# Kernel optimization log

Measured on AMD Instinct MI355X. Metric: run time of the kernel, lower is better.

The kernel has to match this reference:

```python
import jax, jax.numpy as jnp
import numpy as np
from jax import lax

B, CIN, COUT, H, W = 4, 32, 64, 192, 192
K = 3  # kernel size
RED = 16  # SE reduction
EPS = 1e-5


def _conv2d_same(x, w, b):
    y = lax.conv_general_dilated(x, w, (1, 1), 'SAME',
                                 dimension_numbers=('NCHW', 'OIHW', 'NCHW'))
    return y + b[None, :, None, None]


def _bilinear_gather(x, py, px):
    # x: [B,C,H,W]; py/px: [B,KK,H,W] absolute sample coords -> [B,C,KK,H,W]
    Bb, C, Hh, Ww = x.shape
    KK = py.shape[1]
    y0 = jnp.floor(py); x0 = jnp.floor(px)
    wy = py - y0; wx = px - x0
    x_flat = x.reshape(Bb, C, Hh * Ww)

    def corner(yi, xi, wgt):
        valid = (yi >= 0) & (yi < Hh) & (xi >= 0) & (xi < Ww)
        yc = jnp.clip(yi, 0, Hh - 1).astype(jnp.int32)
        xc = jnp.clip(xi, 0, Ww - 1).astype(jnp.int32)
        idx = (yc * Ww + xc).reshape(Bb, 1, KK * Hh * Ww)
        g = jnp.take_along_axis(x_flat, idx, axis=2).reshape(Bb, C, KK, Hh, Ww)
        w_eff = (wgt * valid.astype(x.dtype))[:, None]  # [B,1,KK,H,W]
        return g * w_eff

    out = (corner(y0, x0, (1 - wy) * (1 - wx))
           + corner(y0, x0 + 1, (1 - wy) * wx)
           + corner(y0 + 1, x0, wy * (1 - wx))
           + corner(y0 + 1, x0 + 1, wy * wx))
    return out  # [B,C,KK,H,W]


def _deform_conv(x, offsets, w, b):
    # torchvision DeformConv2d, stride 1, pad 1, dilation 1, 1 offset group.
    Bb, C, Hh, Ww = x.shape
    off = offsets.reshape(Bb, K * K, 2, Hh, Ww)
    dy, dx = off[:, :, 0], off[:, :, 1]  # [B,KK,H,W]
    ky, kx = jnp.meshgrid(jnp.arange(K) - 1, jnp.arange(K) - 1, indexing='ij')
    hg, wg = jnp.meshgrid(jnp.arange(Hh), jnp.arange(Ww), indexing='ij')
    py = hg[None, None] + ky.reshape(-1)[None, :, None, None] + dy
    px = wg[None, None] + kx.reshape(-1)[None, :, None, None] + dx
    sampled = _bilinear_gather(x, py, px)  # [B,CIN,KK,H,W]
    y = jnp.einsum('bckhw,ock->bohw', sampled, w.reshape(w.shape[0], C, K * K))
    return y + b[None, :, None, None]


def _forward(x, w_off, b_off, w_def, b_def, bn_gamma, bn_beta,
             fc1_w, fc1_b, fc2_w, fc2_b):
    offsets = _conv2d_same(x, w_off, b_off)
    y = _deform_conv(x, offsets, w_def, b_def)
    # BatchNorm2d (training-mode batch statistics)
    mean = jnp.mean(y, axis=(0, 2, 3), keepdims=True)
    var = jnp.var(y, axis=(0, 2, 3), keepdims=True)
    y = (y - mean) * lax.rsqrt(var + EPS)
    y = y * bn_gamma[None, :, None, None] + bn_beta[None, :, None, None]
    # SE layer
    s = jnp.mean(y, axis=(2, 3))  # [B,C]
    s = jax.nn.relu(s @ fc1_w.T + fc1_b)
    s = jax.nn.sigmoid(s @ fc2_w.T + fc2_b)
    y = y * s[:, :, None, None]
    y = jax.nn.relu(y)
    # MaxPool 2x2 stride 2
    y = lax.reduce_window(y, -jnp.inf, lax.max, (1, 1, 2, 2), (1, 1, 2, 2), 'VALID')
    return y


def setup_inputs() -> dict:
    key = jax.random.key(0)
    ks = jax.random.split(key, 12)
    rn = lambda k, s, sc=1.0: (jax.random.normal(k, s, dtype=jnp.float32) * sc)
    return {
        'x': rn(ks[0], (B, CIN, H, W)),
        'w_off': rn(ks[1], (2 * K * K, CIN, K, K), 0.02),
        'b_off': jnp.zeros((2 * K * K,), jnp.float32),
        'w_def': rn(ks[2], (COUT, CIN, K, K), 0.05),
        'b_def': rn(ks[3], (COUT,), 0.05),
        'bn_gamma': jnp.ones((COUT,), jnp.float32),
        'bn_beta': jnp.zeros((COUT,), jnp.float32),
        'fc1_w': rn(ks[4], (COUT // RED, COUT), 0.1),
        'fc1_b': jnp.zeros((COUT // RED,), jnp.float32),
        'fc2_w': rn(ks[5], (COUT, COUT // RED), 0.1),
        'fc2_b': jnp.zeros((COUT,), jnp.float32),
    }


def reference(x, w_off, b_off, w_def, b_def, bn_gamma, bn_beta,
              fc1_w, fc1_b, fc2_w, fc2_b):
    return _forward(x, w_off, b_off, w_def, b_def, bn_gamma, bn_beta,
                    fc1_w, fc1_b, fc2_w, fc2_b)
```

## Files before the change

kernel.cpp:

```cpp
#include <hip/hip_runtime.h>
#include <math.h>

#define B_    4
#define CIN_  32
#define COUT_ 64
#define H_    192
#define W_    192
#define HW_   (H_ * W_)
#define NPIX_ (B_ * HW_)
#define EPS_  1e-5f

static __device__ __forceinline__ int swz1152(int blk) {
    return ((blk & 7) * 144) + (blk >> 3);
}

__global__ __launch_bounds__(256) void k_pre(
    const float* __restrict__ x, const float* __restrict__ w_def,
    const float* __restrict__ w_off, float* __restrict__ xt,
    float* __restrict__ wt_def, float* __restrict__ wt_off,
    float* __restrict__ stats)
{
    if (blockIdx.x < NPIX_ / 256) {
        const int pid = blockIdx.x * 256 + threadIdx.x;
        const int b   = pid / HW_;
        const int rem = pid - b * HW_;
        const float* xb = x + (size_t)b * CIN_ * HW_ + rem;
        float4 v[8];
#pragma unroll
        for (int j = 0; j < 8; ++j) {
            v[j].x = xb[(j * 4 + 0) * HW_];
            v[j].y = xb[(j * 4 + 1) * HW_];
            v[j].z = xb[(j * 4 + 2) * HW_];
            v[j].w = xb[(j * 4 + 3) * HW_];
        }
        float4* dst = (float4*)(xt + (size_t)pid * 32);
#pragma unroll
        for (int j = 0; j < 8; ++j) dst[j] = v[j];
    } else {
        const int i = (blockIdx.x - NPIX_ / 256) * 256 + threadIdx.x;
        if (i < 18432) {
            const int o  = i & 63;
            const int c  = (i >> 6) & 31;
            const int kk = i >> 11;
            wt_def[i] = w_def[(o * 32 + c) * 9 + kk];
        } else if (i < 18432 + 5760) {
            const int e  = i - 18432;
            const int o  = e % 20;
            const int t  = e / 20;
            const int c  = t & 31;
            const int kk = t >> 5;
            wt_off[e] = (o < 18) ? w_off[(o * 32 + c) * 9 + kk] : 0.f;
        } else if (i < 18432 + 5760 + 512) {
            stats[i - 18432 - 5760] = 0.f;
        }
    }
}

__global__ __launch_bounds__(128, 4) void k_conv_off(
    const float* __restrict__ xt, const float* __restrict__ wt,
    const float* __restrict__ b_off, float* __restrict__ offs)
{
    const int pid = swz1152(blockIdx.x) * 128 + threadIdx.x;
    const int b   = pid / HW_;
    const int rem = pid - b * HW_;
    const int h   = rem / W_;
    const int w   = rem - h * W_;
    const float* xb = xt + (size_t)b * HW_ * 32;

    float acc[20];
#pragma unroll
    for (int o = 0; o < 20; ++o) acc[o] = 0.f;

#pragma unroll 1
    for (int kk = 0; kk < 9; ++kk) {
        const int yy = h + kk / 3 - 1;
        const int sx = w + kk % 3 - 1;
        const bool ok = (yy >= 0) & (yy < H_) & (sx >= 0) & (sx < W_);
        const int cy = min(max(yy, 0), H_ - 1);
        const int cx = min(max(sx, 0), W_ - 1);
        const float g = ok ? 1.f : 0.f;
        const float* cp = xb + (cy * W_ + cx) * 32;

#pragma unroll 1
        for (int c8 = 0; c8 < 4; ++c8) {
            const float4 x0 = *(const float4*)(cp + c8 * 8);
            const float4 x1 = *(const float4*)(cp + c8 * 8 + 4);
            float vs[8] = {x0.x * g, x0.y * g, x0.z * g, x0.w * g,
                           x1.x * g, x1.y * g, x1.z * g, x1.w * g};
#pragma unroll
            for (int e = 0; e < 8; ++e) {
                const float4* wr = (const float4*)(wt + (kk * 32 + c8 * 8 + e) * 20);
                const float a = vs[e];
#pragma unroll
                for (int q = 0; q < 5; ++q) {
                    float4 wv = wr[q];
                    acc[q * 4 + 0] += a * wv.x;
                    acc[q * 4 + 1] += a * wv.y;
                    acc[q * 4 + 2] += a * wv.z;
                    acc[q * 4 + 3] += a * wv.w;
                }
            }
        }
    }

#pragma unroll
    for (int o = 0; o < 18; ++o)
        offs[(b * 18 + o) * HW_ + rem] = acc[o] + b_off[o];
}

__global__ __launch_bounds__(128, 2) void k_deform(
    const float* __restrict__ xt, const float* __restrict__ offs,
    const float* __restrict__ wt, const float* __restrict__ b_def,
    float* __restrict__ y, float* __restrict__ sum_bc,
    float* __restrict__ sumsq_bc)
{
    const int tid  = threadIdx.x;
    const int lane = tid & 63;
    const int pid  = swz1152(blockIdx.x) * 128 + tid;
    const int b    = pid / HW_;
    const int rem  = pid - b * HW_;
    const int h    = rem / W_;
    const int w    = rem - h * W_;
    const float* xb = xt + (size_t)b * HW_ * 32;
    const float* ob = offs + b * 18 * HW_ + rem;

    float acc[64];
#pragma unroll
    for (int o = 0; o < 64; ++o) acc[o] = 0.f;

    float dy = ob[0];
    float dx = ob[HW_];

#pragma unroll 1
    for (int kk = 0; kk < 9; ++kk) {
        float ndy = 0.f, ndx = 0.f;
        if (kk < 8) {
            ndy = ob[(2 * kk + 2) * HW_];
            ndx = ob[(2 * kk + 3) * HW_];
        }
        const float py = (float)(h + kk / 3 - 1) + dy;
        const float px = (float)(w + kk % 3 - 1) + dx;
        const float y0f = floorf(py), x0f = floorf(px);
        const float wy = py - y0f, wx = px - x0f;
        const int iy0 = (int)y0f, ix0 = (int)x0f;
        const int iy1 = iy0 + 1,  ix1 = ix0 + 1;
        const float vy0 = (iy0 >= 0 && iy0 < H_) ? 1.f : 0.f;
        const float vy1 = (iy1 >= 0 && iy1 < H_) ? 1.f : 0.f;
        const float vx0 = (ix0 >= 0 && ix0 < W_) ? 1.f : 0.f;
        const float vx1 = (ix1 >= 0 && ix1 < W_) ? 1.f : 0.f;
        const float w00 = (1.f - wy) * (1.f - wx) * vy0 * vx0;
        const float w01 = (1.f - wy) * wx * vy0 * vx1;
        const float w10 = wy * (1.f - wx) * vy1 * vx0;
        const float w11 = wy * wx * vy1 * vx1;
        const int cy0 = min(max(iy0, 0), H_ - 1), cy1 = min(max(iy1, 0), H_ - 1);
        const int cx0 = min(max(ix0, 0), W_ - 1), cx1 = min(max(ix1, 0), W_ - 1);
        const int o00 = (cy0 * W_ + cx0) * 32, o01 = (cy0 * W_ + cx1) * 32;
        const int o10 = (cy1 * W_ + cx0) * 32, o11 = (cy1 * W_ + cx1) * 32;

#pragma unroll 1
        for (int c8 = 0; c8 < 4; ++c8) {
            const int co = c8 * 8;
            const float4 a0 = *(const float4*)(xb + o00 + co);
            const float4 b0 = *(const float4*)(xb + o01 + co);
            const float4 c0 = *(const float4*)(xb + o10 + co);
            const float4 d0 = *(const float4*)(xb + o11 + co);
            const float4 a1 = *(const float4*)(xb + o00 + co + 4);
            const float4 b1 = *(const float4*)(xb + o01 + co + 4);
            const float4 c1 = *(const float4*)(xb + o10 + co + 4);
            const float4 d1 = *(const float4*)(xb + o11 + co + 4);
            float v[8];
            v[0] = w00 * a0.x + w01 * b0.x + w10 * c0.x + w11 * d0.x;
            v[1] = w00 * a0.y + w01 * b0.y + w10 * c0.y + w11 * d0.y;
            v[2] = w00 * a0.z + w01 * b0.z + w10 * c0.z + w11 * d0.z;
            v[3] = w00 * a0.w + w01 * b0.w + w10 * c0.w + w11 * d0.w;
            v[4] = w00 * a1.x + w01 * b1.x + w10 * c1.x + w11 * d1.x;
            v[5] = w00 * a1.y + w01 * b1.y + w10 * c1.y + w11 * d1.y;
            v[6] = w00 * a1.z + w01 * b1.z + w10 * c1.z + w11 * d1.z;
            v[7] = w00 * a1.w + w01 * b1.w + w10 * c1.w + w11 * d1.w;
#pragma unroll
            for (int e = 0; e < 8; ++e) {
                const float vc = v[e];
                const float4* wr = (const float4*)(wt + ((kk * 32 + co + e) << 6));
#pragma unroll
                for (int q = 0; q < 16; ++q) {
                    float4 wv = wr[q];
                    acc[q * 4 + 0] += vc * wv.x;
                    acc[q * 4 + 1] += vc * wv.y;
                    acc[q * 4 + 2] += vc * wv.z;
                    acc[q * 4 + 3] += vc * wv.w;
                }
            }
        }
        dy = ndy; dx = ndx;
    }

    float* yp = y + (size_t)b * COUT_ * HW_ + rem;
#pragma unroll
    for (int o = 0; o < 64; ++o) {
        acc[o] += b_def[o];
        yp[o * HW_] = acc[o];
    }

    float ls = 0.f, lq = 0.f;
#pragma unroll
    for (int o = 0; o < 64; ++o) {
        float t = acc[o];
        float u = t * t;
#pragma unroll
        for (int s = 32; s; s >>= 1) {
            t += __shfl_xor(t, s, 64);
            u += __shfl_xor(u, s, 64);
        }
        if (lane == o) { ls = t; lq = u; }
    }
    atomicAdd(&sum_bc[b * 64 + lane], ls);
    atomicAdd(&sumsq_bc[b * 64 + lane], lq);
}

__global__ __launch_bounds__(256) void k_finish(
    const float* __restrict__ y,
    const float* __restrict__ sum_bc, const float* __restrict__ sumsq_bc,
    const float* __restrict__ gamma, const float* __restrict__ beta,
    const float* __restrict__ fc1_w, const float* __restrict__ fc1_b,
    const float* __restrict__ fc2_w, const float* __restrict__ fc2_b,
    float* __restrict__ out)
{
    __shared__ float sal[256], sbb[256], sin_[256];
    const int tid = threadIdx.x;
    {
        const int b = tid >> 6, c = tid & 63;
        float ch_s = 0.f, ch_q = 0.f;
#pragma unroll
        for (int bb = 0; bb < 4; ++bb) {
            ch_s += sum_bc[bb * 64 + c];
            ch_q += sumsq_bc[bb * 64 + c];
        }
        const float invN = 1.f / (float)(B_ * HW_);
        const float mean = ch_s * invN;
        const float var  = ch_q * invN - mean * mean;
        const float a    = gamma[c] * rsqrtf(var + EPS_);
        const float bi   = beta[c] - mean * a;
        sin_[tid] = a * (sum_bc[tid] * (1.f / (float)HW_)) + bi;
        __syncthreads();
        float hv[4];
#pragma unroll
        for (int j = 0; j < 4; ++j) {
            float hs = fc1_b[j];
            for (int cc = 0; cc < 64; ++cc)
                hs += sin_[b * 64 + cc] * fc1_w[j * 64 + cc];
            hv[j] = fmaxf(hs, 0.f);
        }
        float o = fc2_b[c];
#pragma unroll
        for (int j = 0; j < 4; ++j) o += hv[j] * fc2_w[c * 4 + j];
        const float s = 1.f / (1.f + expf(-o));
        sal[tid] = a * s;
        sbb[tid] = bi * s;
    }
    __syncthreads();

    const int t    = blockIdx.x * 256 + tid;
    const int opix = t * 2;
    const int bc   = opix / (96 * 96);
    const int rem  = opix - bc * (96 * 96);
    const int oh   = rem / 96, ow = rem - oh * 96;
    const float al = sal[bc], bb = sbb[bc];
    const float* yp = y + (size_t)bc * HW_ + (2 * oh) * W_ + 2 * ow;
    const float4 r0 = *(const float4*)yp;
    const float4 r1 = *(const float4*)(yp + W_);
    float2 st;
    st.x = fmaxf(fmaxf(fmaxf(fmaf(r0.x, al, bb), fmaf(r0.y, al, bb)),
                       fmaxf(fmaf(r1.x, al, bb), fmaf(r1.y, al, bb))), 0.f);
    st.y = fmaxf(fmaxf(fmaxf(fmaf(r0.z, al, bb), fmaf(r0.w, al, bb)),
                       fmaxf(fmaf(r1.z, al, bb), fmaf(r1.w, al, bb))), 0.f);
    *(float2*)(out + opix) = st;
}

extern "C" void kernel_launch(void* const* d_in, const int* in_sizes, int n_in,
                              void* d_out, int out_size, void* d_ws, size_t ws_size,
                              hipStream_t stream)
{
    const float* x     = (const float*)d_in[0];
    const float* w_off = (const float*)d_in[1];
    const float* b_off = (const float*)d_in[2];
    const float* w_def = (const float*)d_in[3];
    const float* b_def = (const float*)d_in[4];
    const float* gamma = (const float*)d_in[5];
    const float* beta  = (const float*)d_in[6];
    const float* fc1_w = (const float*)d_in[7];
    const float* fc1_b = (const float*)d_in[8];
    const float* fc2_w = (const float*)d_in[9];
    const float* fc2_b = (const float*)d_in[10];
    float* out = (float*)d_out;

    float* ws   = (float*)d_ws;
    float* offs   = ws;
    float* yb     = offs + 2654208;
    float* xt     = yb + 9437184;
    float* wt_def = xt + 4718592;
    float* wt_off = wt_def + 18432;
    float* stats  = wt_off + 5760;
    float* sum_bc   = stats;
    float* sumsq_bc = stats + 256;

    k_pre     <<<dim3(NPIX_ / 256 + 97), dim3(256), 0, stream>>>(
                  x, w_def, w_off, xt, wt_def, wt_off, stats);
    k_conv_off<<<dim3(NPIX_ / 128), dim3(128), 0, stream>>>(xt, wt_off, b_off, offs);
    k_deform  <<<dim3(NPIX_ / 128), dim3(128), 0, stream>>>(xt, offs, wt_def, b_def,
                                                            yb, sum_bc, sumsq_bc);
    k_finish  <<<dim3(B_ * COUT_ * 96 * 96 / 512), dim3(256), 0, stream>>>(
                  yb, sum_bc, sumsq_bc, gamma, beta,
                  fc1_w, fc1_b, fc2_w, fc2_b, out);
}
```

Baseline: 272.4 us.

## Split conv_off and deform work across four thread groups per pixel block

Both convolution kernels now launch 512 threads per 128-pixel block, with four groups of threads per pixel. In conv_off each group handles 8 input channels, and the partial sums are reduced through shared memory. In deform each group gathers 8 channels of bilinear samples into shared memory, then computes 16 of the 64 output channels, with a software-prefetched next tap. The aim is to cut per-thread register pressure (64 accumulators down to 16) and raise occupancy and memory-level parallelism. The cost is extra LDS traffic and two block barriers per tap.

```diff
diff --git a/kernel.cpp b/kernel.cpp
--- a/kernel.cpp
+++ b/kernel.cpp
@@ -13,6 +13,8 @@
 static __device__ __forceinline__ int swz1152(int blk) {
     return ((blk & 7) * 144) + (blk >> 3);
 }
+
+struct Cr { int o00, o01, o10, o11; float w00, w01, w10, w11; };
 
 __global__ __launch_bounds__(256) void k_pre(
     const float* __restrict__ x, const float* __restrict__ w_def,
@@ -56,154 +58,192 @@
     }
 }
 
-__global__ __launch_bounds__(128, 4) void k_conv_off(
+__global__ __launch_bounds__(512, 6) void k_conv_off(
     const float* __restrict__ xt, const float* __restrict__ wt,
     const float* __restrict__ b_off, float* __restrict__ offs)
 {
-    const int pid = swz1152(blockIdx.x) * 128 + threadIdx.x;
+    __shared__ float rlds[4 * 128 * 21];
+    const int tid = threadIdx.x;
+    const int px  = tid & 127;
+    const int grp = __builtin_amdgcn_readfirstlane(tid >> 7);
+    const int pid = swz1152(blockIdx.x) * 128 + px;
     const int b   = pid / HW_;
     const int rem = pid - b * HW_;
     const int h   = rem / W_;
     const int w   = rem - h * W_;
-    const float* xb = xt + (size_t)b * HW_ * 32;
+    const float* xg = xt + (size_t)b * HW_ * 32 + grp * 8;
 
     float acc[20];
 #pragma unroll
     for (int o = 0; o < 20; ++o) acc[o] = 0.f;
 
-#pragma unroll 1
-    for (int kk = 0; kk < 9; ++kk) {
+    auto tapoff = [&](int kk, float& g) -> int {
         const int yy = h + kk / 3 - 1;
         const int sx = w + kk % 3 - 1;
         const bool ok = (yy >= 0) & (yy < H_) & (sx >= 0) & (sx < W_);
+        g = ok ? 1.f : 0.f;
         const int cy = min(max(yy, 0), H_ - 1);
         const int cx = min(max(sx, 0), W_ - 1);
-        const float g = ok ? 1.f : 0.f;
-        const float* cp = xb + (cy * W_ + cx) * 32;
+        return (cy * W_ + cx) * 32;
+    };
+
+    float g; int off = tapoff(0, g);
+    float4 x0 = *(const float4*)(xg + off);
+    float4 x1 = *(const float4*)(xg + off + 4);
 
 #pragma unroll 1
-        for (int c8 = 0; c8 < 4; ++c8) {
-            const float4 x0 = *(const float4*)(cp + c8 * 8);
-            const float4 x1 = *(const float4*)(cp + c8 * 8 + 4);
-            float vs[8] = {x0.x * g, x0.y * g, x0.z * g, x0.w * g,
-                           x1.x * g, x1.y * g, x1.z * g, x1.w * g};
-#pragma unroll
-            for (int e = 0; e < 8; ++e) {
-                const float4* wr = (const float4*)(wt + (kk * 32 + c8 * 8 + e) * 20);
-                const float a = vs[e];
-#pragma unroll
-                for (int q = 0; q < 5; ++q) {
-                    float4 wv = wr[q];
-                    acc[q * 4 + 0] += a * wv.x;
-                    acc[q * 4 + 1] += a * wv.y;
-                    acc[q * 4 + 2] += a * wv.z;
-                    acc[q * 4 + 3] += a * wv.w;
-                }
+    for (int kk = 0; kk < 9; ++kk) {
+        float ng = 0.f; float4 nx0, nx1;
+        if (kk < 8) {
+            const int noff = tapoff(kk + 1, ng);
+            nx0 = *(const float4*)(xg + noff);
+            nx1 = *(const float4*)(xg + noff + 4);
+        }
+        const float vs[8] = {x0.x * g, x0.y * g, x0.z * g, x0.w * g,
+                             x1.x * g, x1.y * g, x1.z * g, x1.w * g};
+#pragma unroll
+        for (int e = 0; e < 8; ++e) {
+            const float4* wr = (const float4*)(wt + (kk * 32 + grp * 8 + e) * 20);
+            const float a = vs[e];
+#pragma unroll
+            for (int q = 0; q < 5; ++q) {
+                float4 wv = wr[q];
+                acc[q * 4 + 0] += a * wv.x;
+                acc[q * 4 + 1] += a * wv.y;
+                acc[q * 4 + 2] += a * wv.z;
+                acc[q * 4 + 3] += a * wv.w;
             }
         }
-    }
-
-#pragma unroll
-    for (int o = 0; o < 18; ++o)
-        offs[(b * 18 + o) * HW_ + rem] = acc[o] + b_off[o];
-}
-
-__global__ __launch_bounds__(128, 2) void k_deform(
+        x0 = nx0; x1 = nx1; g = ng;
+    }
+
+    float* rp = &rlds[(grp * 128 + px) * 21];
+#pragma unroll
+    for (int o = 0; o < 20; ++o) rp[o] = acc[o];
+    __syncthreads();
+
+#pragma unroll
+    for (int j = 0; j < 5; ++j) {
+        const int o = grp * 5 + j;
+        if (o < 18) {
+            const float s = rlds[(0 * 128 + px) * 21 + o]
+                          + rlds[(1 * 128 + px) * 21 + o]
+                          + rlds[(2 * 128 + px) * 21 + o]
+                          + rlds[(3 * 128 + px) * 21 + o];
+            offs[(b * 18 + o) * HW_ + rem] = s + b_off[o];
+        }
+    }
+}
+
+__global__ __launch_bounds__(512, 6) void k_deform(
     const float* __restrict__ xt, const float* __restrict__ offs,
     const float* __restrict__ wt, const float* __restrict__ b_def,
     float* __restrict__ y, float* __restrict__ sum_bc,
     float* __restrict__ sumsq_bc)
 {
+    __shared__ float vlds[32 * 128];
     const int tid  = threadIdx.x;
+    const int px   = tid & 127;
+    const int grp  = __builtin_amdgcn_readfirstlane(tid >> 7);
     const int lane = tid & 63;
-    const int pid  = swz1152(blockIdx.x) * 128 + tid;
+    const int pid  = swz1152(blockIdx.x) * 128 + px;
     const int b    = pid / HW_;
     const int rem  = pid - b * HW_;
     const int h    = rem / W_;
     const int w    = rem - h * W_;
-    const float* xb = xt + (size_t)b * HW_ * 32;
+    const float* xg = xt + (size_t)b * HW_ * 32 + grp * 8;
     const float* ob = offs + b * 18 * HW_ + rem;
 
-    float acc[64];
-#pragma unroll
-    for (int o = 0; o < 64; ++o) acc[o] = 0.f;
-
-    float dy = ob[0];
-    float dx = ob[HW_];
-
-#pragma unroll 1
-    for (int kk = 0; kk < 9; ++kk) {
-        float ndy = 0.f, ndx = 0.f;
-        if (kk < 8) {
-            ndy = ob[(2 * kk + 2) * HW_];
-            ndx = ob[(2 * kk + 3) * HW_];
-        }
+    float acc[16];
+#pragma unroll
+    for (int q = 0; q < 16; ++q) acc[q] = 0.f;
+
+    auto mk = [&](int kk, float dy, float dx) -> Cr {
         const float py = (float)(h + kk / 3 - 1) + dy;
-        const float px = (float)(w + kk % 3 - 1) + dx;
-        const float y0f = floorf(py), x0f = floorf(px);
-        const float wy = py - y0f, wx = px - x0f;
+        const float qx = (float)(w + kk % 3 - 1) + dx;
+        const float y0f = floorf(py), x0f = floorf(qx);
+        const float wy = py - y0f, wx = qx - x0f;
         const int iy0 = (int)y0f, ix0 = (int)x0f;
         const int iy1 = iy0 + 1,  ix1 = ix0 + 1;
         const float vy0 = (iy0 >= 0 && iy0 < H_) ? 1.f : 0.f;
         const float vy1 = (iy1 >= 0 && iy1 < H_) ? 1.f : 0.f;
         const float vx0 = (ix0 >= 0 && ix0 < W_) ? 1.f : 0.f;
         const float vx1 = (ix1 >= 0 && ix1 < W_) ? 1.f : 0.f;
-        const float w00 = (1.f - wy) * (1.f - wx) * vy0 * vx0;
-        const float w01 = (1.f - wy) * wx * vy0 * vx1;
-        const float w10 = wy * (1.f - wx) * vy1 * vx0;
-        const float w11 = wy * wx * vy1 * vx1;
+        Cr c;
+        c.w00 = (1.f - wy) * (1.f - wx) * vy0 * vx0;
+        c.w01 = (1.f - wy) * wx * vy0 * vx1;
+        c.w10 = wy * (1.f - wx) * vy1 * vx0;
+        c.w11 = wy * wx * vy1 * vx1;
         const int cy0 = min(max(iy0, 0), H_ - 1), cy1 = min(max(iy1, 0), H_ - 1);
         const int cx0 = min(max(ix0, 0), W_ - 1), cx1 = min(max(ix1, 0), W_ - 1);
-        const int o00 = (cy0 * W_ + cx0) * 32, o01 = (cy0 * W_ + cx1) * 32;
-        const int o10 = (cy1 * W_ + cx0) * 32, o11 = (cy1 * W_ + cx1) * 32;
+        c.o00 = (cy0 * W_ + cx0) * 32; c.o01 = (cy0 * W_ + cx1) * 32;
+        c.o10 = (cy1 * W_ + cx0) * 32; c.o11 = (cy1 * W_ + cx1) * 32;
+        return c;
+    };
+
+    float dy = ob[0], dx = ob[HW_];
+    Cr cur = mk(0, dy, dx);
+    float4 A0 = *(const float4*)(xg + cur.o00), A1 = *(const float4*)(xg + cur.o00 + 4);
+    float4 B0 = *(const float4*)(xg + cur.o01), B1 = *(const float4*)(xg + cur.o01 + 4);
+    float4 C0 = *(const float4*)(xg + cur.o10), C1 = *(const float4*)(xg + cur.o10 + 4);
+    float4 D0 = *(const float4*)(xg + cur.o11), D1 = *(const float4*)(xg + cur.o11 + 4);
+    float ndy = ob[2 * HW_], ndx = ob[3 * HW_];
 
 #pragma unroll 1
-        for (int c8 = 0; c8 < 4; ++c8) {
-            const int co = c8 * 8;
-            const float4 a0 = *(const float4*)(xb + o00 + co);
-            const float4 b0 = *(const float4*)(xb + o01 + co);
-            const float4 c0 = *(const float4*)(xb + o10 + co);
-            const float4 d0 = *(const float4*)(xb + o11 + co);
-            const float4 a1 = *(const float4*)(xb + o00 + co + 4);
-            const float4 b1 = *(const float4*)(xb + o01 + co + 4);
-            const float4 c1 = *(const float4*)(xb + o10 + co + 4);
-            const float4 d1 = *(const float4*)(xb + o11 + co + 4);
-            float v[8];
-            v[0] = w00 * a0.x + w01 * b0.x + w10 * c0.x + w11 * d0.x;
-            v[1] = w00 * a0.y + w01 * b0.y + w10 * c0.y + w11 * d0.y;
-            v[2] = w00 * a0.z + w01 * b0.z + w10 * c0.z + w11 * d0.z;
-            v[3] = w00 * a0.w + w01 * b0.w + w10 * c0.w + w11 * d0.w;
-            v[4] = w00 * a1.x + w01 * b1.x + w10 * c1.x + w11 * d1.x;
-            v[5] = w00 * a1.y + w01 * b1.y + w10 * c1.y + w11 * d1.y;
-            v[6] = w00 * a1.z + w01 * b1.z + w10 * c1.z + w11 * d1.z;
-            v[7] = w00 * a1.w + w01 * b1.w + w10 * c1.w + w11 * d1.w;
-#pragma unroll
-            for (int e = 0; e < 8; ++e) {
-                const float vc = v[e];
-                const float4* wr = (const float4*)(wt + ((kk * 32 + co + e) << 6));
-#pragma unroll
-                for (int q = 0; q < 16; ++q) {
-                    float4 wv = wr[q];
-                    acc[q * 4 + 0] += vc * wv.x;
-                    acc[q * 4 + 1] += vc * wv.y;
-                    acc[q * 4 + 2] += vc * wv.z;
-                    acc[q * 4 + 3] += vc * wv.w;
-                }
+    for (int kk = 0; kk < 9; ++kk) {
+        __syncthreads();
+        float v[8];
+        v[0] = cur.w00 * A0.x + cur.w01 * B0.x + cur.w10 * C0.x + cur.w11 * D0.x;
+        v[1] = cur.w00 * A0.y + cur.w01 * B0.y + cur.w10 * C0.y + cur.w11 * D0.y;
+        v[2] = cur.w00 * A0.z + cur.w01 * B0.z + cur.w10 * C0.z + cur.w11 * D0.z;
+        v[3] = cur.w00 * A0.w + cur.w01 * B0.w + cur.w10 * C0.w + cur.w11 * D0.w;
+        v[4] = cur.w00 * A1.x + cur.w01 * B1.x + cur.w10 * C1.x + cur.w11 * D1.x;
+        v[5] = cur.w00 * A1.y + cur.w01 * B1.y + cur.w10 * C1.y + cur.w11 * D1.y;
+        v[6] = cur.w00 * A1.z + cur.w01 * B1.z + cur.w10 * C1.z + cur.w11 * D1.z;
+        v[7] = cur.w00 * A1.w + cur.w01 * B1.w + cur.w10 * C1.w + cur.w11 * D1.w;
+#pragma unroll
+        for (int j = 0; j < 8; ++j) vlds[(grp * 8 + j) * 128 + px] = v[j];
+
+        if (kk < 8) {
+            cur = mk(kk + 1, ndy, ndx);
+            A0 = *(const float4*)(xg + cur.o00); A1 = *(const float4*)(xg + cur.o00 + 4);
+            B0 = *(const float4*)(xg + cur.o01); B1 = *(const float4*)(xg + cur.o01 + 4);
+            C0 = *(const float4*)(xg + cur.o10); C1 = *(const float4*)(xg + cur.o10 + 4);
+            D0 = *(const float4*)(xg + cur.o11); D1 = *(const float4*)(xg + cur.o11 + 4);
+            if (kk < 7) {
+                ndy = ob[(2 * kk + 4) * HW_];
+                ndx = ob[(2 * kk + 5) * HW_];
             }
         }
-        dy = ndy; dx = ndx;
-    }
-
-    float* yp = y + (size_t)b * COUT_ * HW_ + rem;
-#pragma unroll
-    for (int o = 0; o < 64; ++o) {
-        acc[o] += b_def[o];
-        yp[o * HW_] = acc[o];
+        __syncthreads();
+
+        const float* wk = wt + (kk << 11) + (grp << 4);
+#pragma unroll 8
+        for (int c = 0; c < 32; ++c) {
+            const float vv = vlds[c * 128 + px];
+            const float4* wr = (const float4*)(wk + (c << 6));
+            const float4 w0 = wr[0], w1 = wr[1], w2 = wr[2], w3 = wr[3];
+            acc[ 0] += vv * w0.x; acc[ 1] += vv * w0.y;
+            acc[ 2] += vv * w0.z; acc[ 3] += vv * w0.w;
+            acc[ 4] += vv * w1.x; acc[ 5] += vv * w1.y;
+            acc[ 6] += vv * w1.z; acc[ 7] += vv * w1.w;
+            acc[ 8] += vv * w2.x; acc[ 9] += vv * w2.y;
+            acc[10] += vv * w2.z; acc[11] += vv * w2.w;
+            acc[12] += vv * w3.x; acc[13] += vv * w3.y;
+            acc[14] += vv * w3.z; acc[15] += vv * w3.w;
+        }
+    }
+
+    float* yp = y + ((size_t)b * COUT_ + grp * 16) * HW_ + rem;
+#pragma unroll
+    for (int q = 0; q < 16; ++q) {
+        acc[q] += b_def[grp * 16 + q];
+        yp[q * HW_] = acc[q];
     }
 
     float ls = 0.f, lq = 0.f;
 #pragma unroll
-    for (int o = 0; o < 64; ++o) {
+    for (int o = 0; o < 16; ++o) {
         float t = acc[o];
         float u = t * t;
 #pragma unroll
@@ -213,8 +253,10 @@
         }
         if (lane == o) { ls = t; lq = u; }
     }
-    atomicAdd(&sum_bc[b * 64 + lane], ls);
-    atomicAdd(&sumsq_bc[b * 64 + lane], lq);
+    if (lane < 16) {
+        atomicAdd(&sum_bc[b * 64 + grp * 16 + lane], ls);
+        atomicAdd(&sumsq_bc[b * 64 + grp * 16 + lane], lq);
+    }
 }
 
 __global__ __launch_bounds__(256) void k_finish(
@@ -305,8 +347,8 @@
 
     k_pre     <<<dim3(NPIX_ / 256 + 97), dim3(256), 0, stream>>>(
                   x, w_def, w_off, xt, wt_def, wt_off, stats);
-    k_conv_off<<<dim3(NPIX_ / 128), dim3(128), 0, stream>>>(xt, wt_off, b_off, offs);
-    k_deform  <<<dim3(NPIX_ / 128), dim3(128), 0, stream>>>(xt, offs, wt_def, b_def,
+    k_conv_off<<<dim3(NPIX_ / 128), dim3(512), 0, stream>>>(xt, wt_off, b_off, offs);
+    k_deform  <<<dim3(NPIX_ / 128), dim3(512), 0, stream>>>(xt, offs, wt_def, b_def,
                                                             yb, sum_bc, sumsq_bc);
     k_finish  <<<dim3(B_ * COUT_ * 96 * 96 / 512), dim3(256), 0, stream>>>(
                   yb, sum_bc, sumsq_bc, gamma, beta,
```

Measured after the change: 248.9 us. 8.6% less time.
